# Optimization experiments

Hardware: AMD Instinct MI355X
Metric: run time of the kernel (lower is better)

## Reference

```python
import jax, jax.numpy as jnp
import numpy as np

LMBDA = 1.0  # init lmbda

def setup_inputs() -> dict:
    key = jax.random.key(0)
    k1, k2, k3 = jax.random.split(key, 3)
    N, P, M = 8, 4096, 2048
    x_hat = jax.random.normal(k1, (N, P, 3), dtype=jnp.float32)
    points = jax.random.normal(k2, (N, P, 3), dtype=jnp.float32)
    # likelihoods in (0, 1]; avoid log2(0)
    lik_y = jax.random.uniform(k3, (N, M), dtype=jnp.float32, minval=1e-6, maxval=1.0)
    return {"x_hat": x_hat, "points": points, "lik_y": lik_y}

def _chamfer(x, y):
    # x: [N,P,3], y: [N,Q,3] -> scalar bidirectional mean chamfer (squared L2)
    x2 = jnp.sum(x * x, axis=-1)                      # [N,P]
    y2 = jnp.sum(y * y, axis=-1)                      # [N,Q]
    xy = jnp.einsum('npc,nqc->npq', x, y)             # [N,P,Q]
    d = x2[:, :, None] + y2[None if False else slice(None), None, :] - 2.0 * xy  # [N,P,Q]
    d = x2[:, :, None] + y2[:, None, :] - 2.0 * xy    # [N,P,Q] squared distances
    cham_x = jnp.mean(jnp.min(d, axis=2))             # x -> nearest in y
    cham_y = jnp.mean(jnp.min(d, axis=1))             # y -> nearest in x
    return cham_x + cham_y

def reference(x_hat, points, lik_y):
    N, P, C = points.shape
    # bpp loss: sum log2(likelihood) / (-N) bits, normalized per point
    bit_y = jnp.sum(jnp.log2(lik_y)) / (-N)
    bpp_y = bit_y / P
    bit_loss = bit_y
    bpp_loss = bit_loss / P
    rec_loss = _chamfer(x_hat, points)
    loss = bpp_loss + LMBDA * rec_loss
    return loss, bpp_loss, rec_loss, bit_loss, bpp_y
```

## Files before the change

### kernel.cpp

```cpp
#include <hip/hip_runtime.h>
#include <math.h>

#define NB 8
#define PP 4096
#define MM 2048
#define DIRS 2
#define QSLICES 16
#define QS (PP / QSLICES)
#define NPTS 8
#define PCHUNK (256 * NPTS)
#define NPBLK (PP / PCHUNK)
#define NMIN (DIRS * NB * PP)
#define NLIK (NB * MM)

typedef float v2f __attribute__((ext_vector_type(2)));

__global__ __launch_bounds__(256, 2) void chamfer_kernel(const float* __restrict__ x,
                                                         const float* __restrict__ y,
                                                         float* __restrict__ wspart) {
    int bx = blockIdx.x;
    int qs  = bx & (QSLICES - 1); bx >>= 4;
    int pc  = bx & (NPBLK - 1);   bx >>= 1;
    int n   = bx & (NB - 1);      bx >>= 3;
    int dir = bx;
    const float* a = dir ? y : x;
    const float* b = dir ? x : y;
    const float* an = a + (size_t)n * PP * 3;
    const float* bn = b + (size_t)n * PP * 3;

    __shared__ float4 lds[QS * 2 / 2 * 2];
    int t = threadIdx.x;

    float X0[NPTS], X1[NPTS], X2[NPTS], XS[NPTS], M[NPTS];
    #pragma unroll
    for (int i = 0; i < NPTS; ++i) {
        int p = pc * PCHUNK + i * 256 + t;
        const float* ap = an + (size_t)p * 3;
        X0[i] = ap[0]; X1[i] = ap[1]; X2[i] = ap[2];
        XS[i] = X0[i] * X0[i] + X1[i] * X1[i] + X2[i] * X2[i];
        M[i] = INFINITY;
    }

    {
        int q = qs * QS + t;
        const float* bp = bn + (size_t)q * 3;
        float y0 = bp[0], y1 = bp[1], y2 = bp[2];
        int j = t >> 1, par = t & 1;
        float* base = (float*)&lds[2 * j];
        base[0 + par] = -2.f * y0;
        base[2 + par] = -2.f * y1;
        base[4 + par] = -2.f * y2;
        base[6 + par] = y0 * y0 + y1 * y1 + y2 * y2;
    }
    __syncthreads();

    #pragma unroll 2
    for (int j = 0; j < QS / 2; ++j) {
        float4 A = lds[2 * j];
        float4 B = lds[2 * j + 1];
        v2f Y0 = {A.x, A.y}, Y1 = {A.z, A.w}, Y2 = {B.x, B.y}, YS = {B.z, B.w};
        #pragma unroll
        for (int i = 0; i < NPTS; ++i) {
            v2f x0 = {X0[i], X0[i]}, x1 = {X1[i], X1[i]}, x2 = {X2[i], X2[i]};
            v2f d = __builtin_elementwise_fma(x0, Y0,
                    __builtin_elementwise_fma(x1, Y1,
                    __builtin_elementwise_fma(x2, Y2, YS)));
            M[i] = fminf(fminf(M[i], d.x), d.y);
        }
    }

    float* plane = wspart + (size_t)qs * NMIN;
    int slot = (dir * NB + n) * PP + pc * PCHUNK + t;
    #pragma unroll
    for (int i = 0; i < NPTS; ++i)
        plane[slot + i * 256] = M[i] + XS[i];
}

__global__ __launch_bounds__(256) void reduce_kernel(const float* __restrict__ wspart,
                                                     const float* __restrict__ lik,
                                                     float* __restrict__ wssum,
                                                     float* __restrict__ out) {
    int t = blockIdx.x * 256 + threadIdx.x;
    float m = wspart[t];
    #pragma unroll
    for (int s = 1; s < QSLICES; ++s)
        m = fminf(m, wspart[(size_t)s * NMIN + t]);

    float l = 0.f;
    if (t < NLIK) l = __log2f(lik[t]);

    #pragma unroll
    for (int off = 32; off > 0; off >>= 1) {
        m += __shfl_down(m, off, 64);
        l += __shfl_down(l, off, 64);
    }
    __shared__ float rm[4], rl[4];
    int lane = threadIdx.x & 63, wid = threadIdx.x >> 6;
    if (lane == 0) { rm[wid] = m; rl[wid] = l; }
    __syncthreads();
    if (threadIdx.x == 0) {
        int dir = blockIdx.x >> 7;
        atomicAdd(&wssum[dir], rm[0] + rm[1] + rm[2] + rm[3]);
        if (blockIdx.x < 64)
            atomicAdd(&wssum[2], rl[0] + rl[1] + rl[2] + rl[3]);
        __threadfence();
        unsigned done = atomicAdd((unsigned*)&wssum[3], 1u);
        if (done == 255u) {
            __threadfence();
            float s0 = __hip_atomic_load(&wssum[0], __ATOMIC_ACQUIRE, __HIP_MEMORY_SCOPE_AGENT);
            float s1 = __hip_atomic_load(&wssum[1], __ATOMIC_ACQUIRE, __HIP_MEMORY_SCOPE_AGENT);
            float s2 = __hip_atomic_load(&wssum[2], __ATOMIC_ACQUIRE, __HIP_MEMORY_SCOPE_AGENT);
            float rec = s0 / (float)(NB * PP) + s1 / (float)(NB * PP);
            float bit_y = s2 / (-(float)NB);
            float bpp = bit_y / (float)PP;
            out[0] = bpp + 1.0f * rec;
            out[1] = bpp;
            out[2] = rec;
            out[3] = bit_y;
            out[4] = bpp;
        }
    }
}

extern "C" void kernel_launch(void* const* d_in, const int* in_sizes, int n_in,
                              void* d_out, int out_size, void* d_ws, size_t ws_size,
                              hipStream_t stream) {
    const float* x_hat  = (const float*)d_in[0];
    const float* points = (const float*)d_in[1];
    const float* lik    = (const float*)d_in[2];
    float* out = (float*)d_out;
    float* wssum  = (float*)d_ws;
    float* wspart = (float*)d_ws + 16;

    hipMemsetAsync(wssum, 0, 16, stream);
    chamfer_kernel<<<DIRS * NB * NPBLK * QSLICES, 256, 0, stream>>>(x_hat, points, wspart);
    reduce_kernel<<<256, 256, 0, stream>>>(wspart, lik, wssum, out);
}
```

Measured before the change: 41.08 us.

## Fuse memset, chamfer and reduction into one cooperative kernel with grid syncs

Replaces the memset and the separate chamfer and reduce launches with one cooperative kernel. Block 0 zeroes the accumulators, all 512 blocks compute the partial minima, a grid-wide sync follows, 256 blocks reduce, a second grid sync follows, and block 0 writes the outputs. This removes two extra launches and the last-block atomic counter. In exchange it pays for a cooperative launch and two grid barriers, and it requires all 512 blocks to be resident at the same time. The LDS array is also trimmed to the size actually used.

```diff
diff --git a/kernel.cpp b/kernel.cpp
--- a/kernel.cpp
+++ b/kernel.cpp
@@ -1,5 +1,8 @@
 #include <hip/hip_runtime.h>
+#include <hip/hip_cooperative_groups.h>
 #include <math.h>
+
+namespace cg = cooperative_groups;
 
 #define NB 8
 #define PP 4096
@@ -10,115 +13,119 @@
 #define NPTS 8
 #define PCHUNK (256 * NPTS)
 #define NPBLK (PP / PCHUNK)
+#define NBLOCKS (DIRS * NB * NPBLK * QSLICES)
 #define NMIN (DIRS * NB * PP)
 #define NLIK (NB * MM)
 
 typedef float v2f __attribute__((ext_vector_type(2)));
 
-__global__ __launch_bounds__(256, 2) void chamfer_kernel(const float* __restrict__ x,
-                                                         const float* __restrict__ y,
-                                                         float* __restrict__ wspart) {
-    int bx = blockIdx.x;
-    int qs  = bx & (QSLICES - 1); bx >>= 4;
-    int pc  = bx & (NPBLK - 1);   bx >>= 1;
-    int n   = bx & (NB - 1);      bx >>= 3;
-    int dir = bx;
-    const float* a = dir ? y : x;
-    const float* b = dir ? x : y;
-    const float* an = a + (size_t)n * PP * 3;
-    const float* bn = b + (size_t)n * PP * 3;
+__global__ __launch_bounds__(256, 2) void fused_kernel(
+        const float* __restrict__ x, const float* __restrict__ y,
+        const float* __restrict__ lik, float* __restrict__ wspart,
+        float* __restrict__ wssum, float* __restrict__ out) {
+    cg::grid_group grid = cg::this_grid();
+    const int t = threadIdx.x;
+    const int bx0 = blockIdx.x;
 
-    __shared__ float4 lds[QS * 2 / 2 * 2];
-    int t = threadIdx.x;
+    if (bx0 == 0 && t < 4) wssum[t] = 0.f;
 
-    float X0[NPTS], X1[NPTS], X2[NPTS], XS[NPTS], M[NPTS];
-    #pragma unroll
-    for (int i = 0; i < NPTS; ++i) {
-        int p = pc * PCHUNK + i * 256 + t;
-        const float* ap = an + (size_t)p * 3;
-        X0[i] = ap[0]; X1[i] = ap[1]; X2[i] = ap[2];
-        XS[i] = X0[i] * X0[i] + X1[i] * X1[i] + X2[i] * X2[i];
-        M[i] = INFINITY;
+    {
+        int bx = bx0;
+        int qs  = bx & (QSLICES - 1); bx >>= 4;
+        int pc  = bx & (NPBLK - 1);   bx >>= 1;
+        int n   = bx & (NB - 1);      bx >>= 3;
+        int dir = bx;
+        const float* a = dir ? y : x;
+        const float* b = dir ? x : y;
+        const float* an = a + (size_t)n * PP * 3;
+        const float* bn = b + (size_t)n * PP * 3;
+
+        __shared__ float4 lds[QS];
+
+        float X0[NPTS], X1[NPTS], X2[NPTS], XS[NPTS], M[NPTS];
+        #pragma unroll
+        for (int i = 0; i < NPTS; ++i) {
+            int p = pc * PCHUNK + i * 256 + t;
+            const float* ap = an + (size_t)p * 3;
+            X0[i] = ap[0]; X1[i] = ap[1]; X2[i] = ap[2];
+            XS[i] = X0[i] * X0[i] + X1[i] * X1[i] + X2[i] * X2[i];
+            M[i] = INFINITY;
+        }
+
+        {
+            int q = qs * QS + t;
+            const float* bp = bn + (size_t)q * 3;
+            float y0 = bp[0], y1 = bp[1], y2 = bp[2];
+            int j = t >> 1, par = t & 1;
+            float* base = (float*)&lds[2 * j];
+            base[0 + par] = -2.f * y0;
+            base[2 + par] = -2.f * y1;
+            base[4 + par] = -2.f * y2;
+            base[6 + par] = y0 * y0 + y1 * y1 + y2 * y2;
+        }
+        __syncthreads();
+
+        #pragma unroll 2
+        for (int j = 0; j < QS / 2; ++j) {
+            float4 A = lds[2 * j];
+            float4 B = lds[2 * j + 1];
+            v2f Y0 = {A.x, A.y}, Y1 = {A.z, A.w}, Y2 = {B.x, B.y}, YS = {B.z, B.w};
+            #pragma unroll
+            for (int i = 0; i < NPTS; ++i) {
+                v2f x0 = {X0[i], X0[i]}, x1 = {X1[i], X1[i]}, x2 = {X2[i], X2[i]};
+                v2f d = __builtin_elementwise_fma(x0, Y0,
+                        __builtin_elementwise_fma(x1, Y1,
+                        __builtin_elementwise_fma(x2, Y2, YS)));
+                M[i] = fminf(fminf(M[i], d.x), d.y);
+            }
+        }
+
+        float* plane = wspart + (size_t)qs * NMIN;
+        int slot = (dir * NB + n) * PP + pc * PCHUNK + t;
+        #pragma unroll
+        for (int i = 0; i < NPTS; ++i)
+            plane[slot + i * 256] = M[i] + XS[i];
     }
 
-    {
-        int q = qs * QS + t;
-        const float* bp = bn + (size_t)q * 3;
-        float y0 = bp[0], y1 = bp[1], y2 = bp[2];
-        int j = t >> 1, par = t & 1;
-        float* base = (float*)&lds[2 * j];
-        base[0 + par] = -2.f * y0;
-        base[2 + par] = -2.f * y1;
-        base[4 + par] = -2.f * y2;
-        base[6 + par] = y0 * y0 + y1 * y1 + y2 * y2;
-    }
-    __syncthreads();
+    grid.sync();
 
-    #pragma unroll 2
-    for (int j = 0; j < QS / 2; ++j) {
-        float4 A = lds[2 * j];
-        float4 B = lds[2 * j + 1];
-        v2f Y0 = {A.x, A.y}, Y1 = {A.z, A.w}, Y2 = {B.x, B.y}, YS = {B.z, B.w};
+    if (bx0 < 256) {
+        int slot = bx0 * 256 + t;
+        float m = wspart[slot];
         #pragma unroll
-        for (int i = 0; i < NPTS; ++i) {
-            v2f x0 = {X0[i], X0[i]}, x1 = {X1[i], X1[i]}, x2 = {X2[i], X2[i]};
-            v2f d = __builtin_elementwise_fma(x0, Y0,
-                    __builtin_elementwise_fma(x1, Y1,
-                    __builtin_elementwise_fma(x2, Y2, YS)));
-            M[i] = fminf(fminf(M[i], d.x), d.y);
+        for (int s = 1; s < QSLICES; ++s)
+            m = fminf(m, wspart[(size_t)s * NMIN + slot]);
+
+        float l = 0.f;
+        if (slot < NLIK) l = __log2f(lik[slot]);
+
+        #pragma unroll
+        for (int off = 32; off > 0; off >>= 1) {
+            m += __shfl_down(m, off, 64);
+            l += __shfl_down(l, off, 64);
+        }
+        __shared__ float rm[4], rl[4];
+        int lane = t & 63, wid = t >> 6;
+        if (lane == 0) { rm[wid] = m; rl[wid] = l; }
+        __syncthreads();
+        if (t == 0) {
+            atomicAdd(&wssum[bx0 >> 7], rm[0] + rm[1] + rm[2] + rm[3]);
+            if (bx0 < 64)
+                atomicAdd(&wssum[2], rl[0] + rl[1] + rl[2] + rl[3]);
         }
     }
 
-    float* plane = wspart + (size_t)qs * NMIN;
-    int slot = (dir * NB + n) * PP + pc * PCHUNK + t;
-    #pragma unroll
-    for (int i = 0; i < NPTS; ++i)
-        plane[slot + i * 256] = M[i] + XS[i];
-}
+    grid.sync();
 
-__global__ __launch_bounds__(256) void reduce_kernel(const float* __restrict__ wspart,
-                                                     const float* __restrict__ lik,
-                                                     float* __restrict__ wssum,
-                                                     float* __restrict__ out) {
-    int t = blockIdx.x * 256 + threadIdx.x;
-    float m = wspart[t];
-    #pragma unroll
-    for (int s = 1; s < QSLICES; ++s)
-        m = fminf(m, wspart[(size_t)s * NMIN + t]);
-
-    float l = 0.f;
-    if (t < NLIK) l = __log2f(lik[t]);
-
-    #pragma unroll
-    for (int off = 32; off > 0; off >>= 1) {
-        m += __shfl_down(m, off, 64);
-        l += __shfl_down(l, off, 64);
-    }
-    __shared__ float rm[4], rl[4];
-    int lane = threadIdx.x & 63, wid = threadIdx.x >> 6;
-    if (lane == 0) { rm[wid] = m; rl[wid] = l; }
-    __syncthreads();
-    if (threadIdx.x == 0) {
-        int dir = blockIdx.x >> 7;
-        atomicAdd(&wssum[dir], rm[0] + rm[1] + rm[2] + rm[3]);
-        if (blockIdx.x < 64)
-            atomicAdd(&wssum[2], rl[0] + rl[1] + rl[2] + rl[3]);
-        __threadfence();
-        unsigned done = atomicAdd((unsigned*)&wssum[3], 1u);
-        if (done == 255u) {
-            __threadfence();
-            float s0 = __hip_atomic_load(&wssum[0], __ATOMIC_ACQUIRE, __HIP_MEMORY_SCOPE_AGENT);
-            float s1 = __hip_atomic_load(&wssum[1], __ATOMIC_ACQUIRE, __HIP_MEMORY_SCOPE_AGENT);
-            float s2 = __hip_atomic_load(&wssum[2], __ATOMIC_ACQUIRE, __HIP_MEMORY_SCOPE_AGENT);
-            float rec = s0 / (float)(NB * PP) + s1 / (float)(NB * PP);
-            float bit_y = s2 / (-(float)NB);
-            float bpp = bit_y / (float)PP;
-            out[0] = bpp + 1.0f * rec;
-            out[1] = bpp;
-            out[2] = rec;
-            out[3] = bit_y;
-            out[4] = bpp;
-        }
+    if (bx0 == 0 && t == 0) {
+        float rec = wssum[0] / (float)(NB * PP) + wssum[1] / (float)(NB * PP);
+        float bit_y = wssum[2] / (-(float)NB);
+        float bpp = bit_y / (float)PP;
+        out[0] = bpp + 1.0f * rec;
+        out[1] = bpp;
+        out[2] = rec;
+        out[3] = bit_y;
+        out[4] = bpp;
     }
 }
 
@@ -129,10 +136,11 @@
     const float* points = (const float*)d_in[1];
     const float* lik    = (const float*)d_in[2];
     float* out = (float*)d_out;
-    float* wssum  = (float*)d_ws;
-    float* wspart = (float*)d_ws + 16;
+    float* wspart = (float*)d_ws;
+    float* wssum  = (float*)d_ws + (size_t)QSLICES * NMIN;
 
-    hipMemsetAsync(wssum, 0, 16, stream);
-    chamfer_kernel<<<DIRS * NB * NPBLK * QSLICES, 256, 0, stream>>>(x_hat, points, wspart);
-    reduce_kernel<<<256, 256, 0, stream>>>(wspart, lik, wssum, out);
+    void* args[] = { (void*)&x_hat, (void*)&points, (void*)&lik,
+                     (void*)&wspart, (void*)&wssum, (void*)&out };
+    hipLaunchCooperativeKernel((void*)fused_kernel, dim3(NBLOCKS), dim3(256),
+                               args, 0, stream);
 }
```

After: 130.4 us. 3.17x slower.

## Precompute packed query points in a prep kernel and read them directly in chamfer loop

Applied to the files above, without the earlier changes.

Adds a prep kernel that packs each point as (-2y0,-2y1,-2y2,|y|^2) into a float4 buffer in the workspace. The chamfer kernel then reads these packed values straight from global memory with uniform addresses instead of staging through LDS with a barrier. It also swaps the packed v2f FMAs for scalar FMAs. This removes the LDS staging and sync, but adds an extra kernel launch and a global write/read pass. Scalar FMA may also lose packed-math throughput, and uniform global loads depend on cache or scalar-load behaviour.

```diff
diff --git a/kernel.cpp b/kernel.cpp
--- a/kernel.cpp
+++ b/kernel.cpp
@@ -13,24 +13,31 @@
 #define NMIN (DIRS * NB * PP)
 #define NLIK (NB * MM)
 
-typedef float v2f __attribute__((ext_vector_type(2)));
+__global__ __launch_bounds__(256) void prep_kernel(const float* __restrict__ x,
+                                                   const float* __restrict__ y,
+                                                   float4* __restrict__ qpack) {
+    int idx = blockIdx.x * 256 + threadIdx.x;
+    int dir = idx >> 15;
+    int nq  = idx & 32767;
+    const float* src = (dir ? x : y) + (size_t)nq * 3;
+    float y0 = src[0], y1 = src[1], y2 = src[2];
+    qpack[idx] = make_float4(-2.f * y0, -2.f * y1, -2.f * y2,
+                             y0 * y0 + y1 * y1 + y2 * y2);
+}
 
 __global__ __launch_bounds__(256, 2) void chamfer_kernel(const float* __restrict__ x,
                                                          const float* __restrict__ y,
+                                                         const float4* __restrict__ qpack,
                                                          float* __restrict__ wspart) {
     int bx = blockIdx.x;
     int qs  = bx & (QSLICES - 1); bx >>= 4;
     int pc  = bx & (NPBLK - 1);   bx >>= 1;
     int n   = bx & (NB - 1);      bx >>= 3;
     int dir = bx;
-    const float* a = dir ? y : x;
-    const float* b = dir ? x : y;
-    const float* an = a + (size_t)n * PP * 3;
-    const float* bn = b + (size_t)n * PP * 3;
+    const float* an = (dir ? y : x) + (size_t)n * PP * 3;
+    const float4* qp = qpack + ((size_t)(dir * NB + n) * PP) + (size_t)qs * QS;
 
-    __shared__ float4 lds[QS * 2 / 2 * 2];
     int t = threadIdx.x;
-
     float X0[NPTS], X1[NPTS], X2[NPTS], XS[NPTS], M[NPTS];
     #pragma unroll
     for (int i = 0; i < NPTS; ++i) {
@@ -41,31 +48,15 @@
         M[i] = INFINITY;
     }
 
-    {
-        int q = qs * QS + t;
-        const float* bp = bn + (size_t)q * 3;
-        float y0 = bp[0], y1 = bp[1], y2 = bp[2];
-        int j = t >> 1, par = t & 1;
-        float* base = (float*)&lds[2 * j];
-        base[0 + par] = -2.f * y0;
-        base[2 + par] = -2.f * y1;
-        base[4 + par] = -2.f * y2;
-        base[6 + par] = y0 * y0 + y1 * y1 + y2 * y2;
-    }
-    __syncthreads();
-
-    #pragma unroll 2
-    for (int j = 0; j < QS / 2; ++j) {
-        float4 A = lds[2 * j];
-        float4 B = lds[2 * j + 1];
-        v2f Y0 = {A.x, A.y}, Y1 = {A.z, A.w}, Y2 = {B.x, B.y}, YS = {B.z, B.w};
+    #pragma unroll 4
+    for (int j = 0; j < QS; j += 2) {
+        float4 A = qp[j];
+        float4 B = qp[j + 1];
         #pragma unroll
         for (int i = 0; i < NPTS; ++i) {
-            v2f x0 = {X0[i], X0[i]}, x1 = {X1[i], X1[i]}, x2 = {X2[i], X2[i]};
-            v2f d = __builtin_elementwise_fma(x0, Y0,
-                    __builtin_elementwise_fma(x1, Y1,
-                    __builtin_elementwise_fma(x2, Y2, YS)));
-            M[i] = fminf(fminf(M[i], d.x), d.y);
+            float d0 = fmaf(X0[i], A.x, fmaf(X1[i], A.y, fmaf(X2[i], A.z, A.w)));
+            float d1 = fmaf(X0[i], B.x, fmaf(X1[i], B.y, fmaf(X2[i], B.z, B.w)));
+            M[i] = fminf(fminf(M[i], d0), d1);
         }
     }
 
@@ -129,10 +120,12 @@
     const float* points = (const float*)d_in[1];
     const float* lik    = (const float*)d_in[2];
     float* out = (float*)d_out;
-    float* wssum  = (float*)d_ws;
-    float* wspart = (float*)d_ws + 16;
+    float*  wspart = (float*)d_ws;
+    float*  wssum  = (float*)d_ws + (size_t)QSLICES * NMIN;
+    float4* qpack  = (float4*)((float*)d_ws + (size_t)QSLICES * NMIN + 64);
 
     hipMemsetAsync(wssum, 0, 16, stream);
-    chamfer_kernel<<<DIRS * NB * NPBLK * QSLICES, 256, 0, stream>>>(x_hat, points, wspart);
+    prep_kernel<<<NMIN / 256, 256, 0, stream>>>(x_hat, points, qpack);
+    chamfer_kernel<<<DIRS * NB * NPBLK * QSLICES, 256, 0, stream>>>(x_hat, points, qpack, wspart);
     reduce_kernel<<<256, 256, 0, stream>>>(wspart, lik, wssum, out);
 }
```

Result: slower. 51.82 us (+26.2%).
